# Kernel tuning notes

Measured on AMD Instinct MI355X. Metric: run time of the kernel, lower is better.

## Reference

```python
import jax, jax.numpy as jnp
import numpy as np

B, L, D, H, DH = 2, 2048, 768, 12, 3072
HD = D // H          # head dim = 64
EPS = 1e-6
SCALE = float(np.sqrt(HD))


def setup_inputs() -> dict:
    key = jax.random.key(0)
    ks = jax.random.split(key, 24)
    w = lambda k, shape: jax.random.normal(k, shape, jnp.float32) * 0.02
    # RoPE angles: [L, HD//2]
    inv_freq = 1.0 / (10000.0 ** (jnp.arange(HD // 2, dtype=jnp.float32) / (HD // 2)))
    ang = jnp.arange(L, dtype=jnp.float32)[:, None] * inv_freq[None, :]
    return {
        "x": jax.random.normal(ks[0], (B, L, D), jnp.float32),
        "c": jax.random.normal(ks[1], (B, D), jnp.float32),
        "freqs_cos": jnp.cos(ang),
        "freqs_sin": jnp.sin(ang),
        "W_q": w(ks[2], (D, D)), "W_k": w(ks[3], (D, D)),
        "W_v": w(ks[4], (D, D)), "W_o": w(ks[5], (D, D)),
        "cond_w1": w(ks[6], (D, DH)), "cond_b1": jnp.zeros((DH,), jnp.float32),
        "cond_w2": w(ks[7], (DH, D)), "cond_b2": jnp.zeros((D,), jnp.float32),
        "attn_norm_w": jnp.ones((D,), jnp.float32),
        "attn_alpha": w(ks[8], (D, D)), "attn_beta": w(ks[9], (D, D)),
        "attn_gamma": w(ks[10], (D, D)),
        "ffn_gate": w(ks[11], (D, DH)), "ffn_hidden": w(ks[12], (D, DH)),
        "ffn_out": w(ks[13], (DH, D)),
        "ffn_norm_w": jnp.ones((D,), jnp.float32),
        "ffn_beta": w(ks[14], (D, D)), "ffn_gamma": w(ks[15], (D, D)),
    }


def _rms_norm(x, w):
    return w * x * jax.lax.rsqrt(jnp.mean(x * x, axis=-1, keepdims=True) + EPS)


def _rope(x, cos, sin):
    # x: [b, n, l, hd]; complex pairs are consecutive (even, odd) lanes
    x0, x1 = x[..., 0::2], x[..., 1::2]
    c, s = cos[None, None], sin[None, None]          # [1,1,l,hd//2]
    r0 = x0 * c - x1 * s
    r1 = x0 * s + x1 * c
    return jnp.stack([r0, r1], axis=-1).reshape(x.shape)


def _attention(h, cos, sin, W_q, W_k, W_v, W_o):
    b, l, d = h.shape
    split = lambda y: y.reshape(b, l, H, HD).transpose(0, 2, 1, 3)  # b n l hd
    q = _rope(split(h @ W_q), cos, sin)
    k = _rope(split(h @ W_k), cos, sin)
    v = split(h @ W_v)
    scores = jnp.einsum("bnld,bnmd->bnlm", q, k) / SCALE
    attn = jax.nn.softmax(scores, axis=-1)
    o = jnp.einsum("bnlm,bnmd->bnld", attn, v)
    return o.transpose(0, 2, 1, 3).reshape(b, l, d) @ W_o


def reference(x, c, freqs_cos, freqs_sin, W_q, W_k, W_v, W_o,
              cond_w1, cond_b1, cond_w2, cond_b2,
              attn_norm_w, attn_alpha, attn_beta, attn_gamma,
              ffn_gate, ffn_hidden, ffn_out, ffn_norm_w, ffn_beta, ffn_gamma):
    # conditioning embedding
    c2 = jax.nn.silu(c @ cond_w1 + cond_b1) @ cond_w2 + cond_b2   # [b, d]
    mod = lambda W: (c2 @ W)[:, None]                              # [b, 1, d]
    # attention sub-block with AdaLN modulation + alpha gating
    h = _rms_norm(x, attn_norm_w) * mod(attn_gamma) + mod(attn_beta)
    x = x + _attention(h, freqs_cos, freqs_sin, W_q, W_k, W_v, W_o) * mod(attn_alpha)
    # SwiGLU FFN sub-block (original gates the residual by ffn_gamma, not alpha)
    h = _rms_norm(x, ffn_norm_w) * mod(ffn_gamma) + mod(ffn_beta)
    ff = (jax.nn.silu(h @ ffn_gate) * (h @ ffn_hidden)) @ ffn_out
    return x + ff * mod(ffn_gamma)
```

## Files before the change

### kernel.cpp

```cpp
#include <hip/hip_runtime.h>

typedef unsigned short u16;
typedef __attribute__((ext_vector_type(8))) short short8;
typedef __attribute__((ext_vector_type(4))) float f32x4;

#define L_SEQ 2048
#define NHEAD 12
#define KVB 128
#define QBLK 128

__device__ __forceinline__ u16 f2bf(float f) {
    union { float f; unsigned u; } x; x.f = f;
    unsigned r = x.u + 0x7fffu + ((x.u >> 16) & 1u);
    return (u16)(r >> 16);
}
__device__ __forceinline__ float bf2f(u16 u) {
    union { unsigned u; float f; } x; x.u = ((unsigned)u) << 16;
    return x.f;
}
__device__ __forceinline__ float silu_f(float x) { return x / (1.f + __expf(-x)); }

__device__ __forceinline__ void gload16(const u16* g, u16* l) {
    __builtin_amdgcn_global_load_lds(
        (const __attribute__((address_space(1))) void*)g,
        (__attribute__((address_space(3))) void*)l, 16, 0, 0);
}

__global__ __launch_bounds__(256) void transpose_all(
    const float* __restrict__ S0, const float* __restrict__ S1,
    const float* __restrict__ S2, const float* __restrict__ S3,
    const float* __restrict__ S4, const float* __restrict__ S5,
    const float* __restrict__ S6,
    u16* __restrict__ D0, u16* __restrict__ D1, u16* __restrict__ D2,
    u16* __restrict__ D3, u16* __restrict__ D4, u16* __restrict__ D5,
    u16* __restrict__ D6)
{
    int id = blockIdx.x;
    const float* W; u16* Wt; int K, N, local;
    if (id < 2304) {
        int sec = id / 576; local = id - sec * 576; K = 768; N = 768;
        W  = (sec == 0) ? S0 : (sec == 1) ? S1 : (sec == 2) ? S2 : S3;
        Wt = (sec == 0) ? D0 : (sec == 1) ? D1 : (sec == 2) ? D2 : D3;
    } else if (id < 6912) {
        int sec = (id - 2304) / 2304; local = (id - 2304) - sec * 2304; K = 768; N = 3072;
        W = sec ? S5 : S4; Wt = sec ? D5 : D4;
    } else {
        local = id - 6912; K = 3072; N = 768; W = S6; Wt = D6;
    }
    int nx = N >> 5;
    int n0 = (local % nx) * 32, k0 = (local / nx) * 32;
    __shared__ float t[32][33];
    int tx = threadIdx.x & 31, ty = threadIdx.x >> 5;
#pragma unroll
    for (int i = 0; i < 4; i++)
        t[ty + 8 * i][tx] = W[(size_t)(k0 + ty + 8 * i) * N + n0 + tx];
    __syncthreads();
#pragma unroll
    for (int i = 0; i < 4; i++)
        Wt[(size_t)(n0 + ty + 8 * i) * K + k0 + tx] = f2bf(t[tx][ty + 8 * i]);
}

__global__ __launch_bounds__(256) void cond_mlp1(
    const float* __restrict__ c, const float* __restrict__ w1, float* __restrict__ part)
{
    int j = blockIdx.x * 256 + threadIdx.x;
    int d0 = blockIdx.y * 96;
    float a0 = 0.f, a1 = 0.f;
    for (int d = d0; d < d0 + 96; ++d) {
        float w = w1[(size_t)d * 3072 + j];
        a0 += c[d] * w;
        a1 += c[768 + d] * w;
    }
    part[(size_t)(blockIdx.y * 2 + 0) * 3072 + j] = a0;
    part[(size_t)(blockIdx.y * 2 + 1) * 3072 + j] = a1;
}

__global__ __launch_bounds__(256) void cond_mlp2(
    const float* __restrict__ part, const float* __restrict__ b1,
    const float* __restrict__ w2, float* __restrict__ c2part)
{
    __shared__ float hid[2][384];
    const int tid = threadIdx.x;
    const int d0 = blockIdx.y * 384;
    for (int i = tid; i < 768; i += 256) {
        int b = i / 384, dd = i - b * 384;
        float s = b1[d0 + dd];
#pragma unroll
        for (int p = 0; p < 8; p++) s += part[(size_t)(p * 2 + b) * 3072 + d0 + dd];
        hid[b][dd] = silu_f(s);
    }
    __syncthreads();
    int jj = tid & 63, kc = tid >> 6;
    int j = blockIdx.x * 64 + jj;
    float a0 = 0.f, a1 = 0.f;
    for (int dd = kc * 96; dd < kc * 96 + 96; ++dd) {
        float w = w2[(size_t)(d0 + dd) * 768 + j];
        a0 += hid[0][dd] * w;
        a1 += hid[1][dd] * w;
    }
    __shared__ float r0[256], r1[256];
    r0[tid] = a0; r1[tid] = a1;
    __syncthreads();
    if (kc == 0) {
        a0 = r0[jj] + r0[64 + jj] + r0[128 + jj] + r0[192 + jj];
        a1 = r1[jj] + r1[64 + jj] + r1[128 + jj] + r1[192 + jj];
        c2part[(size_t)(blockIdx.y * 2 + 0) * 768 + j] = a0;
        c2part[(size_t)(blockIdx.y * 2 + 1) * 768 + j] = a1;
    }
}

__global__ __launch_bounds__(256) void mod_gemm(
    const float* __restrict__ c2part, const float* __restrict__ b2,
    const float* __restrict__ W0, const float* __restrict__ W1,
    const float* __restrict__ W2, const float* __restrict__ W3,
    const float* __restrict__ W4, float* __restrict__ out)
{
    __shared__ float c2s[2][768];
    const int tid = threadIdx.x;
    for (int i = tid; i < 1536; i += 256) {
        int b = i / 768, d = i - b * 768;
        float s = b2[d];
#pragma unroll
        for (int p = 0; p < 8; p++) s += c2part[(size_t)(p * 2 + b) * 768 + d];
        c2s[b][d] = s;
    }
    __syncthreads();
    int w = blockIdx.y;
    const float* W = (w == 0) ? W0 : (w == 1) ? W1 : (w == 2) ? W2 : (w == 3) ? W3 : W4;
    int jj = tid & 63, kc = tid >> 6;
    int j = blockIdx.x * 64 + jj;
    float a0 = 0.f, a1 = 0.f;
    for (int d = kc * 192; d < kc * 192 + 192; ++d) {
        float ww = W[(size_t)d * 768 + j];
        a0 += c2s[0][d] * ww;
        a1 += c2s[1][d] * ww;
    }
    __shared__ float r0[256], r1[256];
    r0[tid] = a0; r1[tid] = a1;
    __syncthreads();
    if (kc == 0) {
        a0 = r0[jj] + r0[64 + jj] + r0[128 + jj] + r0[192 + jj];
        a1 = r1[jj] + r1[64 + jj] + r1[128 + jj] + r1[192 + jj];
        out[(size_t)(w * 2 + 0) * 768 + j] = a0;
        out[(size_t)(w * 2 + 1) * 768 + j] = a1;
    }
}

__global__ __launch_bounds__(256) void rmsnorm_mod(
    const float* __restrict__ xin, const float* __restrict__ nw,
    const float* __restrict__ gamma, const float* __restrict__ beta,
    u16* __restrict__ hout)
{
    int row = blockIdx.x;
    int b = row >> 11;
    const float* xr = xin + (size_t)row * 768;
    int t = threadIdx.x;
    float v0 = xr[t], v1 = xr[t + 256], v2 = xr[t + 512];
    float ss = v0 * v0 + v1 * v1 + v2 * v2;
#pragma unroll
    for (int m = 1; m < 64; m <<= 1) ss += __shfl_xor(ss, m);
    __shared__ float red[4];
    if ((t & 63) == 0) red[t >> 6] = ss;
    __syncthreads();
    float tot = red[0] + red[1] + red[2] + red[3];
    float rr = rsqrtf(tot * (1.f / 768.f) + 1e-6f);
    u16* ho = hout + (size_t)row * 768;
    const float* g = gamma + (size_t)b * 768;
    const float* be = beta + (size_t)b * 768;
#pragma unroll
    for (int i = 0; i < 3; i++) {
        int col = t + i * 256;
        float v = (i == 0) ? v0 : (i == 1) ? v1 : v2;
        ho[col] = f2bf(v * rr * nw[col] * g[col] + be[col]);
    }
}


__global__ __launch_bounds__(256) void gemm_qkv_rope(
    const u16* __restrict__ A, const u16* __restrict__ Bt,
    const float* __restrict__ fc, const float* __restrict__ fs,
    u16* __restrict__ qo, u16* __restrict__ ko, u16* __restrict__ vraw,
    int M, int N, int K)
{
    const float QSCALE = 0.125f * 1.44269504f;
    __shared__ __align__(16) u16 As[2][128 * 64];
    __shared__ __align__(16) u16 Bs[2][128 * 64];
    const int tid = threadIdx.x;
    const int lane = tid & 63, wid = tid >> 6;
    const int lo = lane & 15, hi = lane >> 4;
    const int bm = blockIdx.x * 128, bn = blockIdx.y * 128;
    const int wrow = (wid >> 1) * 64, wcol = (wid & 1) * 64;

    f32x4 acc[4][4];
#pragma unroll
    for (int a = 0; a < 4; a++)
#pragma unroll
        for (int b = 0; b < 4; b++)
            acc[a][b] = (f32x4){0.f, 0.f, 0.f, 0.f};

    auto stage = [&](int buf, int k0) {
#pragma unroll
        for (int p = 0; p < 4; p++) {
            int ch = tid + p * 256;
            int r = ch >> 3, g = ch & 7;
            gload16(A + (size_t)(bm + r) * K + k0 + ((g ^ (r & 7)) * 8), &As[buf][ch * 8]);
        }
#pragma unroll
        for (int p = 0; p < 4; p++) {
            int ch = tid + p * 256;
            int r = ch >> 3, g = ch & 7;
            gload16(Bt + (size_t)(bn + r) * K + k0 + ((g ^ (r & 7)) * 8), &Bs[buf][ch * 8]);
        }
    };

    stage(0, 0);
    int cur = 0;
    const int NT = K >> 6;
    for (int t = 0; t < NT; t++) {
        __syncthreads();
        if (t + 1 < NT) stage(cur ^ 1, (t + 1) * 64);
        short8 af[4][2], bfr[4][2];
#pragma unroll
        for (int mi = 0; mi < 4; mi++) {
            int r = wrow + mi * 16 + lo;
#pragma unroll
            for (int h = 0; h < 2; h++)
                af[mi][h] = *(const short8*)(&As[cur][r * 64 + (((h * 4 + hi) ^ (r & 7)) * 8)]);
        }
#pragma unroll
        for (int nj = 0; nj < 4; nj++) {
            int r = wcol + nj * 16 + lo;
#pragma unroll
            for (int h = 0; h < 2; h++)
                bfr[nj][h] = *(const short8*)(&Bs[cur][r * 64 + (((h * 4 + hi) ^ (r & 7)) * 8)]);
        }
        __builtin_amdgcn_s_setprio(1);
#pragma unroll
        for (int mi = 0; mi < 4; mi++)
#pragma unroll
            for (int nj = 0; nj < 4; nj++) {
                acc[mi][nj] = __builtin_amdgcn_mfma_f32_16x16x32_bf16(af[mi][0], bfr[nj][0], acc[mi][nj], 0, 0, 0);
                acc[mi][nj] = __builtin_amdgcn_mfma_f32_16x16x32_bf16(af[mi][1], bfr[nj][1], acc[mi][nj], 0, 0, 0);
            }
        __builtin_amdgcn_s_setprio(0);
        cur ^= 1;
    }
    const int which = bn / 768;
#pragma unroll
    for (int mi = 0; mi < 4; mi++)
#pragma unroll
        for (int nj = 0; nj < 4; nj++)
#pragma unroll
            for (int i = 0; i < 4; i++) {
                int row = bm + wrow + mi * 16 + hi * 4 + i;
                int col = bn + wcol + nj * 16 + lo;
                float v = acc[mi][nj][i];
                if (which == 2) {
                    vraw[(size_t)row * 768 + (col - 1536)] = f2bf(v);
                } else {
                    int within = col - which * 768;
                    int h = within >> 6, d = within & 63;
                    int l = row & (L_SEQ - 1), b = row >> 11;
                    int dp = d >> 1;
                    float cc = fc[l * 32 + dp], sn = fs[l * 32 + dp];
                    float pv = __shfl_xor(v, 1);
                    float r_;
                    if ((lo & 1) == 0) r_ = v * cc - pv * sn;
                    else               r_ = pv * sn + v * cc;
                    if (which == 0) r_ *= QSCALE;
                    u16* dst = (which == 0) ? qo : ko;
                    dst[(((size_t)(b * NHEAD + h)) * L_SEQ + l) * 64 + d] = f2bf(r_);
                }
            }
}

__global__ __launch_bounds__(256) void gemm_res64(
    const u16* __restrict__ A, const u16* __restrict__ Bt,
    float* __restrict__ Cf, const float* __restrict__ X, const float* __restrict__ coef,
    int M, int N, int K)
{
    __shared__ __align__(16) u16 As[2][64 * 64];
    __shared__ __align__(16) u16 Bs[2][128 * 64];
    const int tid = threadIdx.x;
    const int lane = tid & 63, wid = tid >> 6;
    const int lo = lane & 15, hi = lane >> 4;
    const int bm = blockIdx.x * 64, bn = blockIdx.y * 128;
    const int wrow = (wid >> 1) * 32, wcol = (wid & 1) * 64;

    f32x4 acc[2][4];
#pragma unroll
    for (int a = 0; a < 2; a++)
#pragma unroll
        for (int b = 0; b < 4; b++)
            acc[a][b] = (f32x4){0.f, 0.f, 0.f, 0.f};

    auto stage = [&](int buf, int k0) {
#pragma unroll
        for (int p = 0; p < 2; p++) {
            int ch = tid + p * 256;
            int r = ch >> 3, g = ch & 7;
            gload16(A + (size_t)(bm + r) * K + k0 + ((g ^ (r & 7)) * 8), &As[buf][ch * 8]);
        }
#pragma unroll
        for (int p = 0; p < 4; p++) {
            int ch = tid + p * 256;
            int r = ch >> 3, g = ch & 7;
            gload16(Bt + (size_t)(bn + r) * K + k0 + ((g ^ (r & 7)) * 8), &Bs[buf][ch * 8]);
        }
    };

    stage(0, 0);
    int cur = 0;
    const int NT = K >> 6;
    for (int t = 0; t < NT; t++) {
        __syncthreads();
        if (t + 1 < NT) stage(cur ^ 1, (t + 1) * 64);
        short8 af[2][2], bfr[4][2];
#pragma unroll
        for (int mi = 0; mi < 2; mi++) {
            int r = wrow + mi * 16 + lo;
#pragma unroll
            for (int h = 0; h < 2; h++)
                af[mi][h] = *(const short8*)(&As[cur][r * 64 + (((h * 4 + hi) ^ (r & 7)) * 8)]);
        }
#pragma unroll
        for (int nj = 0; nj < 4; nj++) {
            int r = wcol + nj * 16 + lo;
#pragma unroll
            for (int h = 0; h < 2; h++)
                bfr[nj][h] = *(const short8*)(&Bs[cur][r * 64 + (((h * 4 + hi) ^ (r & 7)) * 8)]);
        }
        __builtin_amdgcn_s_setprio(1);
#pragma unroll
        for (int mi = 0; mi < 2; mi++)
#pragma unroll
            for (int nj = 0; nj < 4; nj++) {
                acc[mi][nj] = __builtin_amdgcn_mfma_f32_16x16x32_bf16(af[mi][0], bfr[nj][0], acc[mi][nj], 0, 0, 0);
                acc[mi][nj] = __builtin_amdgcn_mfma_f32_16x16x32_bf16(af[mi][1], bfr[nj][1], acc[mi][nj], 0, 0, 0);
            }
        __builtin_amdgcn_s_setprio(0);
        cur ^= 1;
    }
#pragma unroll
    for (int mi = 0; mi < 2; mi++)
#pragma unroll
        for (int nj = 0; nj < 4; nj++)
#pragma unroll
            for (int i = 0; i < 4; i++) {
                int row = bm + wrow + mi * 16 + hi * 4 + i;
                int col = bn + wcol + nj * 16 + lo;
                size_t idx = (size_t)row * N + col;
                int b = row >> 11;
                Cf[idx] = X[idx] + acc[mi][nj][i] * coef[(size_t)b * N + col];
            }
}

__global__ __launch_bounds__(256) void gemm_ffn1(
    const u16* __restrict__ A, const u16* __restrict__ Gt, const u16* __restrict__ Ht,
    u16* __restrict__ ff, int M, int N, int K)
{
    __shared__ __align__(16) u16 As[2][128 * 64];
    __shared__ __align__(16) u16 Gs[2][64 * 64];
    __shared__ __align__(16) u16 Hs[2][64 * 64];
    const int tid = threadIdx.x;
    const int lane = tid & 63, wid = tid >> 6;
    const int lo = lane & 15, hi = lane >> 4;
    const int bm = blockIdx.x * 128, bn = blockIdx.y * 64;
    const int wrow = (wid >> 1) * 64, wcol = (wid & 1) * 32;

    f32x4 ag[4][2], ah[4][2];
#pragma unroll
    for (int a = 0; a < 4; a++)
#pragma unroll
        for (int b = 0; b < 2; b++) {
            ag[a][b] = (f32x4){0.f, 0.f, 0.f, 0.f};
            ah[a][b] = (f32x4){0.f, 0.f, 0.f, 0.f};
        }

    auto stage = [&](int buf, int k0) {
#pragma unroll
        for (int p = 0; p < 4; p++) {
            int ch = tid + p * 256;
            int r = ch >> 3, g = ch & 7;
            gload16(A + (size_t)(bm + r) * K + k0 + ((g ^ (r & 7)) * 8), &As[buf][ch * 8]);
        }
#pragma unroll
        for (int p = 0; p < 2; p++) {
            int ch = tid + p * 256;
            int r = ch >> 3, g = ch & 7;
            gload16(Gt + (size_t)(bn + r) * K + k0 + ((g ^ (r & 7)) * 8), &Gs[buf][ch * 8]);
        }
#pragma unroll
        for (int p = 0; p < 2; p++) {
            int ch = tid + p * 256;
            int r = ch >> 3, g = ch & 7;
            gload16(Ht + (size_t)(bn + r) * K + k0 + ((g ^ (r & 7)) * 8), &Hs[buf][ch * 8]);
        }
    };

    stage(0, 0);
    int cur = 0;
    const int NT = K >> 6;
    for (int t = 0; t < NT; t++) {
        __syncthreads();
        if (t + 1 < NT) stage(cur ^ 1, (t + 1) * 64);
        short8 af[4][2], gf[2][2], hf[2][2];
#pragma unroll
        for (int mi = 0; mi < 4; mi++) {
            int r = wrow + mi * 16 + lo;
#pragma unroll
            for (int h = 0; h < 2; h++)
                af[mi][h] = *(const short8*)(&As[cur][r * 64 + (((h * 4 + hi) ^ (r & 7)) * 8)]);
        }
#pragma unroll
        for (int nj = 0; nj < 2; nj++) {
            int r = wcol + nj * 16 + lo;
#pragma unroll
            for (int h = 0; h < 2; h++) {
                gf[nj][h] = *(const short8*)(&Gs[cur][r * 64 + (((h * 4 + hi) ^ (r & 7)) * 8)]);
                hf[nj][h] = *(const short8*)(&Hs[cur][r * 64 + (((h * 4 + hi) ^ (r & 7)) * 8)]);
            }
        }
        __builtin_amdgcn_s_setprio(1);
#pragma unroll
        for (int mi = 0; mi < 4; mi++)
#pragma unroll
            for (int nj = 0; nj < 2; nj++) {
                ag[mi][nj] = __builtin_amdgcn_mfma_f32_16x16x32_bf16(af[mi][0], gf[nj][0], ag[mi][nj], 0, 0, 0);
                ag[mi][nj] = __builtin_amdgcn_mfma_f32_16x16x32_bf16(af[mi][1], gf[nj][1], ag[mi][nj], 0, 0, 0);
                ah[mi][nj] = __builtin_amdgcn_mfma_f32_16x16x32_bf16(af[mi][0], hf[nj][0], ah[mi][nj], 0, 0, 0);
                ah[mi][nj] = __builtin_amdgcn_mfma_f32_16x16x32_bf16(af[mi][1], hf[nj][1], ah[mi][nj], 0, 0, 0);
            }
        __builtin_amdgcn_s_setprio(0);
        cur ^= 1;
    }
#pragma unroll
    for (int mi = 0; mi < 4; mi++)
#pragma unroll
        for (int nj = 0; nj < 2; nj++)
#pragma unroll
            for (int i = 0; i < 4; i++) {
                int row = bm + wrow + mi * 16 + hi * 4 + i;
                int col = bn + wcol + nj * 16 + lo;
                ff[(size_t)row * N + col] = f2bf(silu_f(ag[mi][nj][i]) * ah[mi][nj][i]);
            }
}

__global__ __launch_bounds__(256) void v_transpose(
    const u16* __restrict__ vr, u16* __restrict__ vt)
{
    __shared__ u16 Vl[64 * 64];
    const int tid = threadIdx.x;
    const int bh = blockIdx.y, lt = blockIdx.x;
    const int b = bh / NHEAD, h = bh % NHEAD;
    const int l0 = lt * 64;
    const int lrow = tid >> 2, ch = tid & 3;
    const size_t srow = ((size_t)(b * L_SEQ + l0 + lrow)) * 768 + h * 64 + ch * 16;
    union { int4 v4[2]; u16 s[16]; } iv;
    iv.v4[0] = *(const int4*)(vr + srow); iv.v4[1] = *(const int4*)(vr + srow + 8);
#pragma unroll
    for (int e = 0; e < 16; e++) {
        int d = ch * 16 + e;
        Vl[d * 64 + (lrow ^ (((d >> 3) & 7) << 3))] = iv.s[e];
    }
    __syncthreads();
    const int d = tid >> 2;
    const int key = ((d >> 3) & 7) << 3;
    int4 o0 = *(const int4*)(&Vl[d * 64 + ((ch * 16) ^ key)]);
    int4 o1 = *(const int4*)(&Vl[d * 64 + ((ch * 16 + 8) ^ key)]);
    u16* vd = vt + ((size_t)bh * 64 + d) * L_SEQ + l0 + ch * 16;
    *(int4*)(vd) = o0; *(int4*)(vd + 8) = o1;
}

__global__ __launch_bounds__(512) void attn_fwd(
    const u16* __restrict__ q, const u16* __restrict__ k, const u16* __restrict__ vt,
    u16* __restrict__ outp)
{
    __shared__ __align__(16) u16 Kb[KVB * 64];
    __shared__ __align__(16) u16 Vb[64 * KVB];
    __shared__ __align__(16) u16 Ps[8][16 * KVB];
    const int tid = threadIdx.x;
    const int lane = tid & 63, wid = tid >> 6;
    const int lo = lane & 15, hi = lane >> 4;
    const int lid = blockIdx.x;
    const int xcd = lid & 7, li = lid >> 3;
    const int bh = xcd * 3 + (li >> 4);
    const int qt = li & 15;
    const int b = bh / NHEAD, h = bh % NHEAD;
    const int q0 = qt * QBLK + wid * 16;
    const u16* qb = q + ((size_t)bh * L_SEQ + q0) * 64;
    const u16* kbase = k + (size_t)bh * L_SEQ * 64;
    const u16* vbase = vt + (size_t)bh * 64 * L_SEQ;

    short8 qa0 = *(const short8*)(qb + lo * 64 + hi * 8);
    short8 qa1 = *(const short8*)(qb + lo * 64 + 32 + hi * 8);

    f32x4 oacc[4];
#pragma unroll
    for (int dt = 0; dt < 4; dt++) oacc[dt] = (f32x4){0.f, 0.f, 0.f, 0.f};
    float m_ = -1e30f, ls = 0.f;

    const int rk = tid >> 3, gk = tid & 7;
    const u16* ka = kbase + (size_t)rk * 64 + ((gk ^ (rk & 7)) * 8);
    const int rv = tid >> 4, gv = tid & 15;
    const u16* va = vbase + (size_t)rv * L_SEQ + ((gv ^ (rv & 15)) * 8);
    u16* kdst = &Kb[tid * 8];
    u16* vdst = &Vb[tid * 8];

    int4 kr0, kr1, vr0, vr1;
    kr0 = *(const int4*)(ka);
    kr1 = *(const int4*)(ka + 4096);
    vr0 = *(const int4*)(va);
    vr1 = *(const int4*)(va + 65536);

    const int NT = L_SEQ / KVB;
    u16* pw = &Ps[wid][0];
    const int pkey = lo << 3;
    for (int t = 0; t < NT; t++) {
        __syncthreads();
        *(int4*)(kdst)        = kr0;
        *(int4*)(kdst + 4096) = kr1;
        *(int4*)(vdst)        = vr0;
        *(int4*)(vdst + 4096) = vr1;
        __syncthreads();
        if (t + 1 < NT) {
            int kv0 = (t + 1) * KVB;
            const u16* kan = ka + (size_t)kv0 * 64;
            const u16* van = va + kv0;
            kr0 = *(const int4*)(kan);
            kr1 = *(const int4*)(kan + 4096);
            vr0 = *(const int4*)(van);
            vr1 = *(const int4*)(van + 65536);
        }
        f32x4 s[8];
#pragma unroll
        for (int nt = 0; nt < 8; nt++) {
            int kr_ = nt * 16 + lo;
            const u16* kp = &Kb[kr_ * 64];
            int key = (kr_ & 7) << 3;
            short8 kf0 = *(const short8*)(kp + ((hi * 8) ^ key));
            short8 kf1 = *(const short8*)(kp + ((32 + hi * 8) ^ key));
            __builtin_amdgcn_s_setprio(1);
            f32x4 z = (f32x4){0.f, 0.f, 0.f, 0.f};
            z = __builtin_amdgcn_mfma_f32_16x16x32_bf16(kf0, qa0, z, 0, 0, 0);
            s[nt] = __builtin_amdgcn_mfma_f32_16x16x32_bf16(kf1, qa1, s[nt] = z, 0, 0, 0);
            __builtin_amdgcn_s_setprio(0);
        }
        float t0 = fmaxf(fmaxf(s[0][0], s[0][1]), fmaxf(s[0][2], s[0][3]));
        float t1 = fmaxf(fmaxf(s[1][0], s[1][1]), fmaxf(s[1][2], s[1][3]));
        float t2 = fmaxf(fmaxf(s[2][0], s[2][1]), fmaxf(s[2][2], s[2][3]));
        float t3 = fmaxf(fmaxf(s[3][0], s[3][1]), fmaxf(s[3][2], s[3][3]));
        float t4 = fmaxf(fmaxf(s[4][0], s[4][1]), fmaxf(s[4][2], s[4][3]));
        float t5 = fmaxf(fmaxf(s[5][0], s[5][1]), fmaxf(s[5][2], s[5][3]));
        float t6 = fmaxf(fmaxf(s[6][0], s[6][1]), fmaxf(s[6][2], s[6][3]));
        float t7 = fmaxf(fmaxf(s[7][0], s[7][1]), fmaxf(s[7][2], s[7][3]));
        float pmax = fmaxf(fmaxf(fmaxf(t0, t1), fmaxf(t2, t3)),
                           fmaxf(fmaxf(t4, t5), fmaxf(t6, t7)));
        pmax = fmaxf(pmax, __shfl_xor(pmax, 16));
        pmax = fmaxf(pmax, __shfl_xor(pmax, 32));
        if (!__all(pmax - m_ <= 8.f)) {
            float mn = fmaxf(m_, pmax);
            float al = exp2f(m_ - mn);
            m_ = mn;
            ls *= al;
#pragma unroll
            for (int dt = 0; dt < 4; dt++) oacc[dt] *= al;
        }
        float rsA = 0.f, rsB = 0.f, rsC = 0.f, rsD = 0.f;
#pragma unroll
        for (int nt = 0; nt < 8; nt++) {
            float p0 = exp2f(s[nt][0] - m_);
            float p1 = exp2f(s[nt][1] - m_);
            float p2 = exp2f(s[nt][2] - m_);
            float p3 = exp2f(s[nt][3] - m_);
            s[nt][0] = p0; s[nt][1] = p1; s[nt][2] = p2; s[nt][3] = p3;
            rsA += p0; rsB += p1; rsC += p2; rsD += p3;
        }
        ls += (rsA + rsB) + (rsC + rsD);
#pragma unroll
        for (int nt = 0; nt < 8; nt++) {
            unsigned w0, w1;
            asm("v_cvt_pk_bf16_f32 %0, %1, %2" : "=v"(w0) : "v"(s[nt][0]), "v"(s[nt][1]));
            asm("v_cvt_pk_bf16_f32 %0, %1, %2" : "=v"(w1) : "v"(s[nt][2]), "v"(s[nt][3]));
            uint2 pk2; pk2.x = w0; pk2.y = w1;
            *(uint2*)(pw + lo * KVB + ((nt * 16 + hi * 4) ^ pkey)) = pk2;
        }
        short8 pa0 = *(const short8*)(pw + lo * KVB + ((0 * 32 + hi * 8) ^ pkey));
        short8 pa1 = *(const short8*)(pw + lo * KVB + ((1 * 32 + hi * 8) ^ pkey));
        short8 pa2 = *(const short8*)(pw + lo * KVB + ((2 * 32 + hi * 8) ^ pkey));
        short8 pa3 = *(const short8*)(pw + lo * KVB + ((3 * 32 + hi * 8) ^ pkey));
#pragma unroll
        for (int dt = 0; dt < 4; dt++) {
            int vr_ = dt * 16 + lo;
            const u16* vp = &Vb[vr_ * KVB];
            int vkey = (vr_ & 15) << 3;
            short8 vf0 = *(const short8*)(vp + ((0 * 32 + hi * 8) ^ vkey));
            short8 vf1 = *(const short8*)(vp + ((1 * 32 + hi * 8) ^ vkey));
            short8 vf2 = *(const short8*)(vp + ((2 * 32 + hi * 8) ^ vkey));
            short8 vf3 = *(const short8*)(vp + ((3 * 32 + hi * 8) ^ vkey));
            __builtin_amdgcn_s_setprio(1);
            oacc[dt] = __builtin_amdgcn_mfma_f32_16x16x32_bf16(vf0, pa0, oacc[dt], 0, 0, 0);
            oacc[dt] = __builtin_amdgcn_mfma_f32_16x16x32_bf16(vf1, pa1, oacc[dt], 0, 0, 0);
            oacc[dt] = __builtin_amdgcn_mfma_f32_16x16x32_bf16(vf2, pa2, oacc[dt], 0, 0, 0);
            oacc[dt] = __builtin_amdgcn_mfma_f32_16x16x32_bf16(vf3, pa3, oacc[dt], 0, 0, 0);
            __builtin_amdgcn_s_setprio(0);
        }
    }
    ls += __shfl_xor(ls, 16);
    ls += __shfl_xor(ls, 32);
    float inv = 1.f / ls;
    int qrow = q0 + lo;
    u16* orow = outp + ((size_t)(b * L_SEQ + qrow)) * 768 + h * 64;
#pragma unroll
    for (int dt = 0; dt < 4; dt++) {
        unsigned w0, w1;
        float o0 = oacc[dt][0] * inv, o1 = oacc[dt][1] * inv;
        float o2 = oacc[dt][2] * inv, o3 = oacc[dt][3] * inv;
        asm("v_cvt_pk_bf16_f32 %0, %1, %2" : "=v"(w0) : "v"(o0), "v"(o1));
        asm("v_cvt_pk_bf16_f32 %0, %1, %2" : "=v"(w1) : "v"(o2), "v"(o3));
        uint2 pk2; pk2.x = w0; pk2.y = w1;
        *(uint2*)(orow + dt * 16 + hi * 4) = pk2;
    }
}

extern "C" void kernel_launch(void* const* d_in, const int* in_sizes, int n_in,
                              void* d_out, int out_size, void* d_ws, size_t ws_size,
                              hipStream_t stream)
{
    const float* x      = (const float*)d_in[0];
    const float* c      = (const float*)d_in[1];
    const float* fcos   = (const float*)d_in[2];
    const float* fsin   = (const float*)d_in[3];
    const float* Wq     = (const float*)d_in[4];
    const float* Wk     = (const float*)d_in[5];
    const float* Wv     = (const float*)d_in[6];
    const float* Wo     = (const float*)d_in[7];
    const float* cw1    = (const float*)d_in[8];
    const float* cb1    = (const float*)d_in[9];
    const float* cw2    = (const float*)d_in[10];
    const float* cb2    = (const float*)d_in[11];
    const float* anw    = (const float*)d_in[12];
    const float* Walpha = (const float*)d_in[13];
    const float* Wbeta  = (const float*)d_in[14];
    const float* Wgamma = (const float*)d_in[15];
    const float* Wgate  = (const float*)d_in[16];
    const float* Whid   = (const float*)d_in[17];
    const float* Wout   = (const float*)d_in[18];
    const float* fnw    = (const float*)d_in[19];
    const float* Wbetaf = (const float*)d_in[20];
    const float* Wgammaf= (const float*)d_in[21];

    const int M = 4096;
    char* ws = (char*)d_ws;
    size_t off = 0;
    auto alloc = [&](size_t bytes) -> char* {
        char* p = ws + off;
        off += (bytes + 255) & ~(size_t)255;
        return p;
    };
    u16* wq_t   = (u16*)alloc((size_t)768 * 768 * 2);
    u16* wk_t   = (u16*)alloc((size_t)768 * 768 * 2);
    u16* wv_t   = (u16*)alloc((size_t)768 * 768 * 2);
    u16* wo_t   = (u16*)alloc((size_t)768 * 768 * 2);
    u16* gate_t = (u16*)alloc((size_t)3072 * 768 * 2);
    u16* hid_t  = (u16*)alloc((size_t)3072 * 768 * 2);
    u16* out_t  = (u16*)alloc((size_t)768 * 3072 * 2);
    float* part1 = (float*)alloc((size_t)8 * 2 * 3072 * 4);
    float* part2 = (float*)alloc((size_t)8 * 2 * 768 * 4);
    float* mods = (float*)alloc(5 * 2 * 768 * 4);
    u16* hbuf   = (u16*)alloc((size_t)M * 768 * 2);
    u16* vraw   = (u16*)alloc((size_t)M * 768 * 2);
    u16* qrope  = (u16*)alloc((size_t)M * 768 * 2);
    u16* krope  = (u16*)alloc((size_t)M * 768 * 2);
    u16* vtb    = (u16*)alloc((size_t)M * 768 * 2);
    u16* attnh  = (u16*)alloc((size_t)M * 768 * 2);
    float* ybuf = (float*)alloc((size_t)M * 768 * 4);
    u16* ffbuf  = (u16*)alloc((size_t)M * 3072 * 2);

    transpose_all<<<9216, 256, 0, stream>>>(
        Wq, Wk, Wv, Wo, Wgate, Whid, Wout,
        wq_t, wk_t, wv_t, wo_t, gate_t, hid_t, out_t);

    cond_mlp1<<<dim3(12, 8), 256, 0, stream>>>(c, cw1, part1);
    cond_mlp2<<<dim3(12, 8), 256, 0, stream>>>(part1, cb1, cw2, part2);
    mod_gemm<<<dim3(12, 5), 256, 0, stream>>>(
        part2, cb2, Wgamma, Wbeta, Walpha, Wgammaf, Wbetaf, mods);

    rmsnorm_mod<<<M, 256, 0, stream>>>(x, anw, mods + 0 * 1536, mods + 1 * 1536, hbuf);

    gemm_qkv_rope<<<dim3(32, 18), 256, 0, stream>>>(
        hbuf, wq_t, fcos, fsin, qrope, krope, vraw, M, 2304, 768);

    v_transpose<<<dim3(32, 24), 256, 0, stream>>>(vraw, vtb);

    attn_fwd<<<dim3(384), 512, 0, stream>>>(qrope, krope, vtb, attnh);

    gemm_res64<<<dim3(64, 6), 256, 0, stream>>>(
        attnh, wo_t, ybuf, x, mods + 2 * 1536, M, 768, 768);

    rmsnorm_mod<<<M, 256, 0, stream>>>(ybuf, fnw, mods + 3 * 1536, mods + 4 * 1536, hbuf);

    gemm_ffn1<<<dim3(32, 48), 256, 0, stream>>>(
        hbuf, gate_t, hid_t, ffbuf, M, 3072, 768);

    gemm_res64<<<dim3(64, 6), 256, 0, stream>>>(
        ffbuf, out_t, (float*)d_out, ybuf, mods + 3 * 1536, M, 768, 3072);
}
```

Measured before the change: 252.0 us.

## Fuse V transpose into QKV GEMM epilogue and store residual in bf16

```diff
diff --git a/kernel.cpp b/kernel.cpp
--- a/kernel.cpp
+++ b/kernel.cpp
@@ -146,16 +146,23 @@
     }
 }
 
+template<int IN>
 __global__ __launch_bounds__(256) void rmsnorm_mod(
-    const float* __restrict__ xin, const float* __restrict__ nw,
+    const void* __restrict__ xin, const float* __restrict__ nw,
     const float* __restrict__ gamma, const float* __restrict__ beta,
     u16* __restrict__ hout)
 {
     int row = blockIdx.x;
     int b = row >> 11;
-    const float* xr = xin + (size_t)row * 768;
     int t = threadIdx.x;
-    float v0 = xr[t], v1 = xr[t + 256], v2 = xr[t + 512];
+    float v0, v1, v2;
+    if (IN == 0) {
+        const float* xr = (const float*)xin + (size_t)row * 768;
+        v0 = xr[t]; v1 = xr[t + 256]; v2 = xr[t + 512];
+    } else {
+        const u16* xr = (const u16*)xin + (size_t)row * 768;
+        v0 = bf2f(xr[t]); v1 = bf2f(xr[t + 256]); v2 = bf2f(xr[t + 512]);
+    }
     float ss = v0 * v0 + v1 * v1 + v2 * v2;
 #pragma unroll
     for (int m = 1; m < 64; m <<= 1) ss += __shfl_xor(ss, m);
@@ -179,7 +186,7 @@
 __global__ __launch_bounds__(256) void gemm_qkv_rope(
     const u16* __restrict__ A, const u16* __restrict__ Bt,
     const float* __restrict__ fc, const float* __restrict__ fs,
-    u16* __restrict__ qo, u16* __restrict__ ko, u16* __restrict__ vraw,
+    u16* __restrict__ qo, u16* __restrict__ ko, u16* __restrict__ vt,
     int M, int N, int K)
 {
     const float QSCALE = 0.125f * 1.44269504f;
@@ -246,18 +253,32 @@
         cur ^= 1;
     }
     const int which = bn / 768;
-#pragma unroll
-    for (int mi = 0; mi < 4; mi++)
-#pragma unroll
-        for (int nj = 0; nj < 4; nj++)
-#pragma unroll
-            for (int i = 0; i < 4; i++) {
-                int row = bm + wrow + mi * 16 + hi * 4 + i;
+    if (which == 2) {
+#pragma unroll
+        for (int mi = 0; mi < 4; mi++)
+#pragma unroll
+            for (int nj = 0; nj < 4; nj++) {
+                int row0 = bm + wrow + mi * 16 + hi * 4;
                 int col = bn + wcol + nj * 16 + lo;
-                float v = acc[mi][nj][i];
-                if (which == 2) {
-                    vraw[(size_t)row * 768 + (col - 1536)] = f2bf(v);
-                } else {
+                int within = col - 1536;
+                int h = within >> 6, d = within & 63;
+                int l0 = row0 & (L_SEQ - 1), b = row0 >> 11;
+                unsigned w0, w1;
+                asm("v_cvt_pk_bf16_f32 %0, %1, %2" : "=v"(w0) : "v"(acc[mi][nj][0]), "v"(acc[mi][nj][1]));
+                asm("v_cvt_pk_bf16_f32 %0, %1, %2" : "=v"(w1) : "v"(acc[mi][nj][2]), "v"(acc[mi][nj][3]));
+                uint2 pk2; pk2.x = w0; pk2.y = w1;
+                *(uint2*)(vt + (((size_t)(b * NHEAD + h)) * 64 + d) * L_SEQ + l0) = pk2;
+            }
+    } else {
+#pragma unroll
+        for (int mi = 0; mi < 4; mi++)
+#pragma unroll
+            for (int nj = 0; nj < 4; nj++)
+#pragma unroll
+                for (int i = 0; i < 4; i++) {
+                    int row = bm + wrow + mi * 16 + hi * 4 + i;
+                    int col = bn + wcol + nj * 16 + lo;
+                    float v = acc[mi][nj][i];
                     int within = col - which * 768;
                     int h = within >> 6, d = within & 63;
                     int l = row & (L_SEQ - 1), b = row >> 11;
@@ -271,12 +292,13 @@
                     u16* dst = (which == 0) ? qo : ko;
                     dst[(((size_t)(b * NHEAD + h)) * L_SEQ + l) * 64 + d] = f2bf(r_);
                 }
-            }
-}
-
+    }
+}
+
+template<int MODE>
 __global__ __launch_bounds__(256) void gemm_res64(
     const u16* __restrict__ A, const u16* __restrict__ Bt,
-    float* __restrict__ Cf, const float* __restrict__ X, const float* __restrict__ coef,
+    void* __restrict__ outp, const void* __restrict__ X, const float* __restrict__ coef,
     int M, int N, int K)
 {
     __shared__ __align__(16) u16 As[2][64 * 64];
@@ -351,7 +373,11 @@
                 int col = bn + wcol + nj * 16 + lo;
                 size_t idx = (size_t)row * N + col;
                 int b = row >> 11;
-                Cf[idx] = X[idx] + acc[mi][nj][i] * coef[(size_t)b * N + col];
+                float base = (MODE == 0) ? ((const float*)X)[idx]
+                                         : bf2f(((const u16*)X)[idx]);
+                float v = base + acc[mi][nj][i] * coef[(size_t)b * N + col];
+                if (MODE == 0) ((u16*)outp)[idx] = f2bf(v);
+                else           ((float*)outp)[idx] = v;
             }
 }
 
@@ -444,32 +470,6 @@
                 int col = bn + wcol + nj * 16 + lo;
                 ff[(size_t)row * N + col] = f2bf(silu_f(ag[mi][nj][i]) * ah[mi][nj][i]);
             }
-}
-
-__global__ __launch_bounds__(256) void v_transpose(
-    const u16* __restrict__ vr, u16* __restrict__ vt)
-{
-    __shared__ u16 Vl[64 * 64];
-    const int tid = threadIdx.x;
-    const int bh = blockIdx.y, lt = blockIdx.x;
-    const int b = bh / NHEAD, h = bh % NHEAD;
-    const int l0 = lt * 64;
-    const int lrow = tid >> 2, ch = tid & 3;
-    const size_t srow = ((size_t)(b * L_SEQ + l0 + lrow)) * 768 + h * 64 + ch * 16;
-    union { int4 v4[2]; u16 s[16]; } iv;
-    iv.v4[0] = *(const int4*)(vr + srow); iv.v4[1] = *(const int4*)(vr + srow + 8);
-#pragma unroll
-    for (int e = 0; e < 16; e++) {
-        int d = ch * 16 + e;
-        Vl[d * 64 + (lrow ^ (((d >> 3) & 7) << 3))] = iv.s[e];
-    }
-    __syncthreads();
-    const int d = tid >> 2;
-    const int key = ((d >> 3) & 7) << 3;
-    int4 o0 = *(const int4*)(&Vl[d * 64 + ((ch * 16) ^ key)]);
-    int4 o1 = *(const int4*)(&Vl[d * 64 + ((ch * 16 + 8) ^ key)]);
-    u16* vd = vt + ((size_t)bh * 64 + d) * L_SEQ + l0 + ch * 16;
-    *(int4*)(vd) = o0; *(int4*)(vd + 8) = o1;
 }
 
 __global__ __launch_bounds__(512) void attn_fwd(
@@ -669,12 +669,11 @@
     float* part2 = (float*)alloc((size_t)8 * 2 * 768 * 4);
     float* mods = (float*)alloc(5 * 2 * 768 * 4);
     u16* hbuf   = (u16*)alloc((size_t)M * 768 * 2);
-    u16* vraw   = (u16*)alloc((size_t)M * 768 * 2);
     u16* qrope  = (u16*)alloc((size_t)M * 768 * 2);
     u16* krope  = (u16*)alloc((size_t)M * 768 * 2);
     u16* vtb    = (u16*)alloc((size_t)M * 768 * 2);
     u16* attnh  = (u16*)alloc((size_t)M * 768 * 2);
-    float* ybuf = (float*)alloc((size_t)M * 768 * 4);
+    u16* ybuf   = (u16*)alloc((size_t)M * 768 * 2);
     u16* ffbuf  = (u16*)alloc((size_t)M * 3072 * 2);
 
     transpose_all<<<9216, 256, 0, stream>>>(
@@ -686,23 +685,21 @@
     mod_gemm<<<dim3(12, 5), 256, 0, stream>>>(
         part2, cb2, Wgamma, Wbeta, Walpha, Wgammaf, Wbetaf, mods);
 
-    rmsnorm_mod<<<M, 256, 0, stream>>>(x, anw, mods + 0 * 1536, mods + 1 * 1536, hbuf);
+    rmsnorm_mod<0><<<M, 256, 0, stream>>>(x, anw, mods + 0 * 1536, mods + 1 * 1536, hbuf);
 
     gemm_qkv_rope<<<dim3(32, 18), 256, 0, stream>>>(
-        hbuf, wq_t, fcos, fsin, qrope, krope, vraw, M, 2304, 768);
-
-    v_transpose<<<dim3(32, 24), 256, 0, stream>>>(vraw, vtb);
+        hbuf, wq_t, fcos, fsin, qrope, krope, vtb, M, 2304, 768);
 
     attn_fwd<<<dim3(384), 512, 0, stream>>>(qrope, krope, vtb, attnh);
 
-    gemm_res64<<<dim3(64, 6), 256, 0, stream>>>(
+    gemm_res64<0><<<dim3(64, 6), 256, 0, stream>>>(
         attnh, wo_t, ybuf, x, mods + 2 * 1536, M, 768, 768);
 
-    rmsnorm_mod<<<M, 256, 0, stream>>>(ybuf, fnw, mods + 3 * 1536, mods + 4 * 1536, hbuf);
+    rmsnorm_mod<1><<<M, 256, 0, stream>>>(ybuf, fnw, mods + 3 * 1536, mods + 4 * 1536, hbuf);
 
     gemm_ffn1<<<dim3(32, 48), 256, 0, stream>>>(
         hbuf, gate_t, hid_t, ffbuf, M, 3072, 768);
 
-    gemm_res64<<<dim3(64, 6), 256, 0, stream>>>(
-        ffbuf, out_t, (float*)d_out, ybuf, mods + 3 * 1536, M, 768, 3072);
-}
+    gemm_res64<1><<<dim3(64, 6), 256, 0, stream>>>(
+        ffbuf, out_t, d_out, ybuf, mods + 3 * 1536, M, 768, 3072);
+}
```

After: 245.3 us, median of 3. -2.7%, faster.
